# Optimization experiments

Hardware: AMD Instinct MI355X
Metric: run time of the kernel (lower is better)

## Reference

```python
import jax, jax.numpy as jnp
import numpy as np

B, T_IN, T_OUT = 32, 512, 800
N_MEL, ENC, ARNN, DRNN, PRE, ATT, LOCF, LOCK = 80, 512, 1024, 1024, 256, 128, 32, 31


def setup_inputs() -> dict:
    key = jax.random.key(0)
    ks = jax.random.split(key, 24)
    s = 0.02
    d = {
        'memory': jax.random.normal(ks[0], (B, T_IN, ENC), jnp.float32),
        'decoder_inputs': jax.random.normal(ks[1], (B, N_MEL, T_OUT), jnp.float32),
        'prenet_w1': jax.random.normal(ks[2], (PRE, N_MEL)) * s,
        'prenet_w2': jax.random.normal(ks[3], (PRE, PRE)) * s,
        'att_rnn_wih': jax.random.normal(ks[4], (4 * ARNN, PRE + ENC)) * s,
        'att_rnn_whh': jax.random.normal(ks[5], (4 * ARNN, ARNN)) * s,
        'att_rnn_bih': jnp.zeros((4 * ARNN,)),
        'att_rnn_bhh': jnp.zeros((4 * ARNN,)),
        'q_w': jax.random.normal(ks[6], (ATT, ARNN)) * s,
        'mem_w': jax.random.normal(ks[7], (ATT, ENC)) * s,
        'v_w': jax.random.normal(ks[8], (1, ATT)) * s,
        'loc_conv_w': jax.random.normal(ks[9], (LOCF, 2, LOCK)) * s,
        'loc_lin_w': jax.random.normal(ks[10], (ATT, LOCF)) * s,
        'dec_rnn_wih': jax.random.normal(ks[11], (4 * DRNN, ARNN + ENC)) * s,
        'dec_rnn_whh': jax.random.normal(ks[12], (4 * DRNN, DRNN)) * s,
        'dec_rnn_bih': jnp.zeros((4 * DRNN,)),
        'dec_rnn_bhh': jnp.zeros((4 * DRNN,)),
        'proj_w': jax.random.normal(ks[13], (N_MEL, DRNN + ENC)) * s,
        'proj_b': jnp.zeros((N_MEL,)),
        'gate_w': jax.random.normal(ks[14], (1, DRNN + ENC)) * s,
        'gate_b': jnp.zeros((1,)),
    }
    lengths = jax.random.randint(ks[15], (B,), T_IN // 2, T_IN + 1)
    d['memory_lengths'] = lengths.at[0].set(T_IN)  # ensure max length spans memory
    return d


def _lstm_cell(x, h, c, wih, whh, bih, bhh):
    z = x @ wih.T + bih + h @ whh.T + bhh
    i, f, g, o = jnp.split(z, 4, axis=-1)
    c = jax.nn.sigmoid(f) * c + jax.nn.sigmoid(i) * jnp.tanh(g)
    h = jax.nn.sigmoid(o) * jnp.tanh(c)
    return h, c


def reference(memory, decoder_inputs, prenet_w1, prenet_w2,
              att_rnn_wih, att_rnn_whh, att_rnn_bih, att_rnn_bhh,
              q_w, mem_w, v_w, loc_conv_w, loc_lin_w,
              dec_rnn_wih, dec_rnn_whh, dec_rnn_bih, dec_rnn_bhh,
              proj_w, proj_b, gate_w, gate_b, memory_lengths):
    # teacher-forced inputs: go frame + first T_OUT-1 mel frames -> [T_OUT, B, N_MEL]
    frames = jnp.transpose(decoder_inputs, (2, 0, 1))  # [T_OUT, B, N_MEL]
    dec_in = jnp.concatenate([jnp.zeros((1, B, N_MEL), memory.dtype), frames[:-1]], 0)
    # prenet (dropout omitted for deterministic reference)
    x = jax.nn.relu(dec_in @ prenet_w1.T)
    pren = jax.nn.relu(x @ prenet_w2.T)  # [T_OUT, B, PRE]

    pmem = memory @ mem_w.T  # [B, T_IN, ATT]
    valid = jnp.arange(T_IN)[None, :] < memory_lengths[:, None]  # [B, T_IN]

    def step(carry, dec_t):
        ah, ac, dh, dc, aw, awc, actx = carry
        cell_in = jnp.concatenate([dec_t, actx], -1)
        ah, ac = _lstm_cell(cell_in, ah, ac, att_rnn_wih, att_rnn_whh, att_rnn_bih, att_rnn_bhh)
        # location-sensitive attention
        cat = jnp.stack([aw, awc], axis=1)  # [B, 2, T_IN]
        loc = jax.lax.conv_general_dilated(cat, loc_conv_w, (1,), 'SAME',
                                           dimension_numbers=('NCH', 'OIH', 'NCH'))  # [B, LOCF, T_IN]
        loc = jnp.einsum('bct,ac->bta', loc, loc_lin_w)  # [B, T_IN, ATT]
        pq = (ah @ q_w.T)[:, None, :]  # [B, 1, ATT]
        energies = jnp.einsum('bta,a->bt', jnp.tanh(pq + loc + pmem), v_w[0])
        energies = jnp.where(valid, energies, -1e9)
        aw = jax.nn.softmax(energies, axis=1)
        actx = jnp.einsum('bt,btd->bd', aw, memory)
        awc = awc + aw
        din = jnp.concatenate([ah, actx], -1)
        dh, dc = _lstm_cell(din, dh, dc, dec_rnn_wih, dec_rnn_whh, dec_rnn_bih, dec_rnn_bhh)
        dhac = jnp.concatenate([dh, actx], -1)
        mel = dhac @ proj_w.T + proj_b  # [B, N_MEL]
        gate = (dhac @ gate_w.T + gate_b)[:, 0]  # [B]
        return (ah, ac, dh, dc, aw, awc, actx), (mel, gate, aw)

    z = lambda *s: jnp.zeros(s, memory.dtype)
    carry0 = (z(B, ARNN), z(B, ARNN), z(B, DRNN), z(B, DRNN), z(B, T_IN), z(B, T_IN), z(B, ENC))
    _, (mels, gates, aligns) = jax.lax.scan(step, carry0, pren)
    mel_outputs = jnp.transpose(mels, (1, 2, 0))      # [B, N_MEL, T_OUT]
    gate_outputs = jnp.transpose(gates, (1, 0))       # [B, T_OUT]
    alignments = jnp.transpose(aligns, (1, 0, 2))     # [B, T_OUT, T_IN]
    return mel_outputs, gate_outputs, alignments
```

## Files before the change

### kernel.cpp

```cpp
#include <hip/hip_runtime.h>
#include <cstddef>


constexpr size_t WT_ATT = 0;
constexpr size_t WT_DEC = 7340032;
constexpr size_t PREN_O = 17825792;
constexpr size_t PMEMT  = 24379392;
constexpr size_t W1T    = 26476544;
constexpr size_t W2T    = 26497024;
constexpr size_t QWT    = 26562560;
constexpr size_t PWT    = 26693632;
constexpr size_t MEMWT  = 26841088;
constexpr size_t XATT   = 26906624;
constexpr size_t XDEC   = 27021312;
constexpr size_t AH_O   = 27185152;
constexpr size_t AC_O   = 27217920;
constexpr size_t DH_O   = 27250688;
constexpr size_t DC_O   = 27283456;
constexpr size_t AWC_O  = 27316224;
constexpr size_t ACTX_O = 27348992;
constexpr size_t ENER_O = 27381760;
constexpr size_t LOC_O  = 27398144;
constexpr size_t BAR_O  = 27922432;

constexpr size_t MEL_OUT = 0;
constexpr size_t GATE_OUT = 2048000;
constexpr size_t ALIGN_OUT = 2073600;

__device__ __forceinline__ float gload(const float* p_) {
  return __hip_atomic_load(p_, __ATOMIC_RELAXED, __HIP_MEMORY_SCOPE_AGENT);
}
__device__ __forceinline__ void gstore(float* p_, float v) {
  __hip_atomic_store(p_, v, __ATOMIC_RELAXED, __HIP_MEMORY_SCOPE_AGENT);
}

__device__ __forceinline__ void gsync(float* ws, unsigned& epoch) {
  unsigned* cnt = (unsigned*)(ws + BAR_O);
  unsigned* rel = (unsigned*)(ws + BAR_O) + 128;
  __syncthreads();
  const int tid = threadIdx.x, bid = blockIdx.x;
  ++epoch;
  if (tid == 0)
    __hip_atomic_fetch_add(&cnt[(bid & 15) * 8], 1u, __ATOMIC_RELAXED,
                           __HIP_MEMORY_SCOPE_AGENT);
  if (bid == 0) {
    if (tid < 64) {
      const unsigned tgt = epoch * 32u;
      bool done;
      do {
        unsigned v = (tid < 16) ? __hip_atomic_load(&cnt[tid * 8], __ATOMIC_RELAXED,
                                                    __HIP_MEMORY_SCOPE_AGENT)
                                : tgt;
        done = v >= tgt;
        if (!done) __builtin_amdgcn_s_sleep(2);
      } while (__ballot(done) != ~0ull);
      for (int rr = tid; rr < 512; rr += 64)
        __hip_atomic_store(&rel[rr * 8], epoch, __ATOMIC_RELAXED,
                           __HIP_MEMORY_SCOPE_AGENT);
    }
  } else if (tid == 0) {
    while (__hip_atomic_load(&rel[bid * 8], __ATOMIC_RELAXED,
                             __HIP_MEMORY_SCOPE_AGENT) < epoch)
      __builtin_amdgcn_s_sleep(4);
  }
  __syncthreads();
}

__device__ __forceinline__ float sigf(float x) {
  float cx = fminf(fmaxf(x, -30.f), 30.f);
  return 1.f / (1.f + __expf(-cx));
}
__device__ __forceinline__ float tanh_f(float x) {
  float cx = fminf(fmaxf(x, -15.f), 15.f);
  float e = __expf(2.f * cx);
  return (e - 1.f) / (e + 1.f);
}

__device__ __forceinline__ void fused_block(
    const float* __restrict__ X, const int K, const float* __restrict__ WB,
    const int g, const int hh, const float* __restrict__ bih,
    const float* __restrict__ bhh, float* __restrict__ cst,
    float* __restrict__ d0, const int s0, float* __restrict__ d1, const int s1,
    float* __restrict__ d2, const int s2, const int tid,
    float* __restrict__ sm) {
  float* Xs = sm;
  float* Ws = sm + 2560;
  const int cg = tid & 3, bg = (tid >> 2) & 1, ks = tid >> 3;
  float acc[8][8];
#pragma unroll
  for (int ci = 0; ci < 8; ++ci)
#pragma unroll
    for (int bi = 0; bi < 8; ++bi) acc[ci][bi] = 0.f;

  const int nc = K >> 7;
  const int kloc = tid & 127, brow = tid >> 7;
  const float* xb = X + (size_t)brow * K + kloc;
  float px[8];
  float4 pw[4];
#pragma unroll
  for (int i = 0; i < 8; ++i) px[i] = gload(xb + (size_t)(2 * i) * K);
#pragma unroll
  for (int j = 0; j < 4; ++j)
    pw[j] = *(const float4*)(WB + (size_t)tid * 4 + j * 1024);

#pragma unroll 1
  for (int c = 0; c < nc; ++c) {
    __syncthreads();
#pragma unroll
    for (int i = 0; i < 8; ++i) Xs[kloc * 20 + brow + 2 * i] = px[i];
#pragma unroll
    for (int j = 0; j < 4; ++j) {
      const int ff = tid + 256 * j;
      *(float4*)(Ws + (ff >> 3) * 36 + (ff & 7) * 4) = pw[j];
    }
    __syncthreads();
    if (c + 1 < nc) {
      const float* xb2 = xb + (c + 1) * 128;
#pragma unroll
      for (int i = 0; i < 8; ++i) px[i] = gload(xb2 + (size_t)(2 * i) * K);
      const float* wb2 = WB + (size_t)(c + 1) * 4096 + (size_t)tid * 4;
#pragma unroll
      for (int j = 0; j < 4; ++j) pw[j] = *(const float4*)(wb2 + j * 1024);
    }
#pragma unroll
    for (int i = 0; i < 4; ++i) {
      const int k = i * 32 + ks;
      const float4 wA = *(const float4*)(Ws + k * 36 + cg * 8);
      const float4 wBv = *(const float4*)(Ws + k * 36 + cg * 8 + 4);
      const float4 xA = *(const float4*)(Xs + k * 20 + bg * 8);
      const float4 xBv = *(const float4*)(Xs + k * 20 + bg * 8 + 4);
      const float wr[8] = {wA.x, wA.y, wA.z, wA.w, wBv.x, wBv.y, wBv.z, wBv.w};
      const float xr[8] = {xA.x, xA.y, xA.z, xA.w, xBv.x, xBv.y, xBv.z, xBv.w};
#pragma unroll
      for (int ci = 0; ci < 8; ++ci)
#pragma unroll
        for (int bi = 0; bi < 8; ++bi)
          acc[ci][bi] = fmaf(wr[ci], xr[bi], acc[ci][bi]);
    }
  }
#pragma unroll
  for (int ci = 0; ci < 8; ++ci)
#pragma unroll
    for (int bi = 0; bi < 8; ++bi) {
      float v = acc[ci][bi];
      v += __shfl_xor(v, 8);
      v += __shfl_xor(v, 16);
      v += __shfl_xor(v, 32);
      acc[ci][bi] = v;
    }
  __syncthreads();
  float* red = sm;
  float* zs = sm + 2560;
  const int lane = tid & 63, wv = tid >> 6;
  if (lane < 8) {
#pragma unroll
    for (int ci = 0; ci < 8; ++ci)
#pragma unroll
      for (int bi = 0; bi < 8; ++bi)
        red[((bg * 8 + bi) * 32 + cg * 8 + ci) * 5 + wv] = acc[ci][bi];
  }
  __syncthreads();
#pragma unroll
  for (int m = 0; m < 2; ++m) {
    const int o = tid + 256 * m;
    zs[o] = red[o * 5] + red[o * 5 + 1] + red[o * 5 + 2] + red[o * 5 + 3];
  }
  __syncthreads();
  if (tid < 128) {
    const int bb = tid & 15, jj = tid >> 4;
    const int j = g * 8 + jj;
    const int b = hh * 16 + bb;
    const float zi = zs[bb * 32 + jj] + bih[j] + bhh[j];
    const float zf = zs[bb * 32 + 8 + jj] + bih[1024 + j] + bhh[1024 + j];
    const float zg = zs[bb * 32 + 16 + jj] + bih[2048 + j] + bhh[2048 + j];
    const float zo = zs[bb * 32 + 24 + jj] + bih[3072 + j] + bhh[3072 + j];
    const float cp = cst[(size_t)b * 1024 + j];
    const float ct = sigf(zf) * cp + sigf(zi) * tanh_f(zg);
    const float ho = sigf(zo) * tanh_f(ct);
    cst[(size_t)b * 1024 + j] = ct;
    gstore(d0 + (size_t)b * s0 + j, ho);
    if (d1) gstore(d1 + (size_t)b * s1 + j, ho);
    if (d2) gstore(d2 + (size_t)b * s2 + j, ho);
  }
}

__global__ __launch_bounds__(256) void k_small(
    const float* __restrict__ w1, const float* __restrict__ w2,
    const float* __restrict__ qw, const float* __restrict__ memw,
    const float* __restrict__ projw, const float* __restrict__ gatew,
    float* __restrict__ ws) {
  size_t i = (size_t)blockIdx.x * 256 + threadIdx.x;
  if (i < 20480) { size_t j = i & 255, m = i >> 8; ws[W1T + m * 256 + j] = w1[j * 80 + m]; return; }
  i -= 20480;
  if (i < 65536) { size_t j = i & 255, k = i >> 8; ws[W2T + k * 256 + j] = w2[j * 256 + k]; return; }
  i -= 65536;
  if (i < 131072) { size_t j = i & 127, k = i >> 7; ws[QWT + k * 128 + j] = qw[j * 1024 + k]; return; }
  i -= 131072;
  if (i < 65536) { size_t a = i & 127, e = i >> 7; ws[MEMWT + e * 128 + a] = memw[a * 512 + e]; return; }
  i -= 65536;
  if (i < 147456) {
    size_t o = i % 96, k = i / 96;
    float v = 0.f;
    if (o < 80) v = projw[o * 1536 + k];
    else if (o == 80) v = gatew[k];
    ws[PWT + k * 96 + o] = v;
  }
}

__device__ __forceinline__ size_t att_out(int gcol, int kout) {
  const int gate = gcol >> 10, g = (gcol & 1023) >> 3, jj = gcol & 7;
  return WT_ATT + ((size_t)g * 1792 + kout) * 32 + gate * 8 + jj;
}
__device__ __forceinline__ size_t dec_out(int gcol, int kout) {
  const int gate = gcol >> 10, g = (gcol & 1023) >> 3, jj = gcol & 7;
  return WT_DEC + ((size_t)g * 2560 + kout) * 32 + gate * 8 + jj;
}
__global__ __launch_bounds__(256) void k_tr_a_wih(const float* __restrict__ w,
                                                  float* __restrict__ ws) {
  const int i = blockIdx.x * 256 + threadIdx.x;
  const int gcol = i / 768, k = i - gcol * 768;
  ws[att_out(gcol, k)] = w[i];
}
__global__ __launch_bounds__(256) void k_tr_a_whh(const float* __restrict__ w,
                                                  float* __restrict__ ws) {
  const int i = blockIdx.x * 256 + threadIdx.x;
  const int gcol = i >> 10, kin = i & 1023;
  ws[att_out(gcol, 768 + kin)] = w[i];
}
__global__ __launch_bounds__(256) void k_tr_d_wih(const float* __restrict__ w,
                                                  float* __restrict__ ws) {
  const int i = blockIdx.x * 256 + threadIdx.x;
  const int gcol = i / 1536, kin = i - gcol * 1536;
  const int kout = (kin < 1024) ? kin : kin + 1024;
  ws[dec_out(gcol, kout)] = w[i];
}
__global__ __launch_bounds__(256) void k_tr_d_whh(const float* __restrict__ w,
                                                  float* __restrict__ ws) {
  const int i = blockIdx.x * 256 + threadIdx.x;
  const int gcol = i >> 10, kin = i & 1023;
  ws[dec_out(gcol, 1024 + kin)] = w[i];
}

__global__ __launch_bounds__(256) void k_prenet(const float* __restrict__ din,
                                                float* __restrict__ ws) {
  __shared__ float h1[8][257];
  const int tg = blockIdx.x, b = blockIdx.y, j = threadIdx.x;
  float acc[8] = {0, 0, 0, 0, 0, 0, 0, 0};
  for (int m = 0; m < 80; ++m) {
    const float w = ws[W1T + m * 256 + j];
#pragma unroll
    for (int q = 0; q < 8; ++q) {
      const int t = tg * 8 + q;
      const float x = (t > 0) ? din[((size_t)b * 80 + m) * 800 + (t - 1)] : 0.f;
      acc[q] = fmaf(x, w, acc[q]);
    }
  }
#pragma unroll
  for (int q = 0; q < 8; ++q) h1[q][j] = fmaxf(acc[q], 0.f);
  __syncthreads();
  float a2[8] = {0, 0, 0, 0, 0, 0, 0, 0};
  for (int k = 0; k < 256; ++k) {
    const float w = ws[W2T + k * 256 + j];
#pragma unroll
    for (int q = 0; q < 8; ++q) a2[q] = fmaf(h1[q][k], w, a2[q]);
  }
#pragma unroll
  for (int q = 0; q < 8; ++q) {
    const int t = tg * 8 + q;
    ws[PREN_O + ((size_t)t * 32 + b) * 256 + j] = fmaxf(a2[q], 0.f);
  }
}

__global__ __launch_bounds__(256) void k_pmem(const float* __restrict__ mem,
                                              float* __restrict__ ws) {
  __shared__ float mt[16 * 516];
  const int b = blockIdx.x, tc = blockIdx.y, tid = threadIdx.x;
  const int ti0 = tc * 16;
  for (int i = tid; i < 16 * 128; i += 256) {
    const int r = i >> 7, c = i & 127;
    *(float4*)(mt + r * 516 + c * 4) =
        *(const float4*)(mem + ((size_t)b * 512 + ti0 + r) * 512 + c * 4);
  }
  __syncthreads();
  const int a = tid & 127, th = tid >> 7;
  float acc[8] = {0, 0, 0, 0, 0, 0, 0, 0};
  for (int e = 0; e < 512; ++e) {
    const float w = ws[MEMWT + (size_t)e * 128 + a];
#pragma unroll
    for (int q = 0; q < 8; ++q) acc[q] = fmaf(w, mt[(th * 8 + q) * 516 + e], acc[q]);
  }
#pragma unroll
  for (int q = 0; q < 8; ++q)
    ws[PMEMT + ((size_t)b * 128 + a) * 512 + ti0 + th * 8 + q] = acc[q];
}

struct TP {
  const float *mem, *abih, *abhh, *lconv, *llw, *vw, *dbih, *dbhh, *projb, *gateb;
  const int* lens;
  float* ws;
  float* out;
};

__global__ __launch_bounds__(256, 2) void taco_main(TP p) {
  __shared__ float smem[7168];
  float* const ws = p.ws;
  unsigned epoch = 0;
  const int bid = blockIdx.x, tid = threadIdx.x;
  const int r = bid & 255, hh = bid >> 8;

#pragma unroll 1
  for (int t = 0; t <= 800; ++t) {
    const int par = t & 1, nxt = (t + 1) & 1, prv = (t - 1) & 1;
    if (r < 128) {
      if (t < 800)
        fused_block(ws + XATT + (size_t)par * 57344 + (size_t)hh * 16 * 1792,
                    1792, ws + WT_ATT + (size_t)r * 1792 * 32, r, hh,
                    p.abih, p.abhh, ws + AC_O,
                    ws + AH_O, 1024,
                    ws + XATT + (size_t)nxt * 57344 + 768, 1792,
                    ws + XDEC + (size_t)par * 81920, 2560, tid, smem);
    } else {
      if (t > 0)
        fused_block(ws + XDEC + (size_t)prv * 81920 + (size_t)hh * 16 * 2560,
                    2560, ws + WT_DEC + (size_t)(r - 128) * 2560 * 32, r - 128,
                    hh, p.dbih, p.dbhh, ws + DC_O,
                    ws + DH_O, 1024,
                    ws + XDEC + (size_t)par * 81920 + 1024, 2560,
                    nullptr, 0, tid, smem);
    }
    gsync(ws, epoch);

    if (r < 128) {
      if (t < 800) {
        const int b = r >> 2, q8 = ((r & 3) << 1) | hh;
        float* sa = smem;
        float* sloc = smem + 1024;
        float* pqp = smem + 3136;
        float* pq = smem + 3392;
        float* sme = smem + 3520;
#pragma unroll
        for (int i = 0; i < 4; ++i)
          sa[tid + 256 * i] = gload(ws + AH_O + (size_t)b * 1024 + tid + 256 * i);
#pragma unroll
        for (int ii = 0; ii < 8; ++ii) {
          const int flat = tid + 256 * ii;
          sloc[(flat >> 5) * 33 + (flat & 31)] =
              gload(ws + LOC_O + (size_t)b * 16384 + (size_t)q8 * 2048 + flat);
        }
        __syncthreads();
        {
          const int j = tid & 127, kh = tid >> 7;
          const float* qb = ws + QWT + (size_t)kh * 512 * 128 + j;
          const float* ab = sa + kh * 512;
          float a0 = 0, a1 = 0, a2 = 0, a3 = 0;
          for (int k = 0; k < 512; k += 4) {
            a0 = fmaf(qb[(size_t)k * 128], ab[k], a0);
            a1 = fmaf(qb[(size_t)(k + 1) * 128], ab[k + 1], a1);
            a2 = fmaf(qb[(size_t)(k + 2) * 128], ab[k + 2], a2);
            a3 = fmaf(qb[(size_t)(k + 3) * 128], ab[k + 3], a3);
          }
          pqp[tid] = (a0 + a1) + (a2 + a3);
        }
        __syncthreads();
        if (tid < 128) pq[tid] = pqp[tid] + pqp[128 + tid];
        __syncthreads();
        const int ti_l = tid & 63, th = tid >> 6;
        float lr[32];
#pragma unroll
        for (int f = 0; f < 32; ++f) lr[f] = sloc[ti_l * 33 + f];
        const float* pmb = ws + PMEMT + (size_t)b * 65536 +
                           (size_t)(th * 32) * 512 + q8 * 64 + ti_l;
        float acc_e = 0;
#pragma unroll 2
        for (int a0 = 0; a0 < 32; ++a0) {
          const int a = th * 32 + a0;
          float s = pq[a] + pmb[(size_t)a0 * 512];
          const float* la = p.llw + a * 32;
#pragma unroll
          for (int f = 0; f < 32; ++f) s = fmaf(lr[f], la[f], s);
          acc_e = fmaf(p.vw[a], tanh_f(s), acc_e);
        }
        sme[tid] = acc_e;
        __syncthreads();
        if (tid < 64) {
          const int ti = q8 * 64 + tid;
          const float e = sme[tid] + sme[64 + tid] + sme[128 + tid] + sme[192 + tid];
          gstore(ws + ENER_O + (size_t)b * 512 + ti, (ti < p.lens[b]) ? e : -1e9f);
        }
      }
    } else if (r < 160 && hh == 0) {
      if (t > 0) {
        const int b = r - 128;
        float* sx = smem;
        float* sred = smem + 1536;
#pragma unroll
        for (int i = 0; i < 6; ++i) {
          const int flat = tid + 256 * i;
          sx[flat] = (flat < 1024)
                         ? gload(ws + DH_O + (size_t)b * 1024 + flat)
                         : gload(ws + ACTX_O + (size_t)prv * 16384 + (size_t)b * 512 +
                                 (flat - 1024));
        }
        __syncthreads();
        float p0 = 0.f, p1 = 0.f, p2 = 0.f, p3 = 0.f;
        const int o = tid / 3, ks2 = tid - o * 3;
        if (o < 81) {
          const float* wcol = ws + PWT + o;
          const int k0 = ks2 * 512;
          for (int k = k0; k < k0 + 512; k += 4) {
            p0 = fmaf(sx[k], wcol[(size_t)k * 96], p0);
            p1 = fmaf(sx[k + 1], wcol[(size_t)(k + 1) * 96], p1);
            p2 = fmaf(sx[k + 2], wcol[(size_t)(k + 2) * 96], p2);
            p3 = fmaf(sx[k + 3], wcol[(size_t)(k + 3) * 96], p3);
          }
        }
        sred[tid] = (p0 + p1) + (p2 + p3);
        __syncthreads();
        if (tid < 81) {
          float ssum = sred[tid * 3] + sred[tid * 3 + 1] + sred[tid * 3 + 2];
          ssum += (tid < 80) ? p.projb[tid] : p.gateb[0];
          if (tid < 80)
            p.out[MEL_OUT + ((size_t)b * 80 + tid) * 800 + (t - 1)] = ssum;
          else
            p.out[GATE_OUT + (size_t)b * 800 + (t - 1)] = ssum;
        }
      }
    }
    gsync(ws, epoch);

    if (t < 800) {
      const int b = r >> 3, dc16 = ((r & 7) << 1) | hh;
      float* se = smem;
      float* red = smem + 512;
      float* sp = smem + 768;
      float* sc = smem + 1280;
      float* saw = smem + 1536;
      float* sawh = smem + 1600;
      float* slc = smem + 1664;
      se[tid] = gload(ws + ENER_O + (size_t)b * 512 + tid);
      se[256 + tid] = gload(ws + ENER_O + (size_t)b * 512 + 256 + tid);
      for (int i = tid; i < 1984; i += 256) slc[i] = p.lconv[i];
      __syncthreads();
      red[tid] = fmaxf(se[tid], se[256 + tid]);
      __syncthreads();
      for (int s = 128; s > 0; s >>= 1) {
        if (tid < s) red[tid] = fmaxf(red[tid], red[tid + s]);
        __syncthreads();
      }
      const float mx = red[0];
      __syncthreads();
      const float p0 = __expf(se[tid] - mx), p1 = __expf(se[256 + tid] - mx);
      sp[tid] = p0;
      sp[256 + tid] = p1;
      red[tid] = p0 + p1;
      __syncthreads();
      for (int s = 128; s > 0; s >>= 1) {
        if (tid < s) red[tid] += red[tid + s];
        __syncthreads();
      }
      const float inv = 1.f / red[0];
      const int tseg = tid >> 5, dl = tid & 31;
      const int base = dc16 * 32;
      const float* mrow =
          p.mem + ((size_t)b * 512 + tseg * 64) * 512 + base + dl;
      float ca = 0, cb = 0;
      for (int i = 0; i < 64; i += 2) {
        ca = fmaf(sp[tseg * 64 + i], mrow[(size_t)i * 512], ca);
        cb = fmaf(sp[tseg * 64 + i + 1], mrow[(size_t)(i + 1) * 512], cb);
      }
      sc[tid] = ca + cb;
      for (int i = tid; i < 62; i += 256) {
        const int x = base - 15 + i;
        const bool ok = (unsigned)x < 512u;
        const float awx = ok ? sp[x] * inv : 0.f;
        saw[i] = awx;
        sawh[i] = awx + (ok ? gload(ws + AWC_O + (size_t)par * 16384 +
                                    (size_t)b * 512 + x)
                            : 0.f);
      }
      __syncthreads();
      if (tid < 32) {
        float v = sc[tid] + sc[32 + tid] + sc[64 + tid] + sc[96 + tid] +
                  sc[128 + tid] + sc[160 + tid] + sc[192 + tid] + sc[224 + tid];
        v *= inv;
        const int dd = base + tid;
        gstore(ws + ACTX_O + (size_t)par * 16384 + (size_t)b * 512 + dd, v);
        gstore(ws + XATT + (size_t)nxt * 57344 + (size_t)b * 1792 + 256 + dd, v);
        gstore(ws + XDEC + (size_t)par * 81920 + (size_t)b * 2560 + 2048 + dd, v);
        gstore(ws + AWC_O + (size_t)nxt * 16384 + (size_t)b * 512 + dd,
               sawh[15 + tid]);
        p.out[ALIGN_OUT + ((size_t)b * 800 + t) * 512 + dd] = sp[dd] * inv;
      }
      if (t + 1 < 800) {
        const int f = tid & 31, tig = tid >> 5;
#pragma unroll 2
        for (int tt = 0; tt < 4; ++tt) {
          const int til = tig + tt * 8;
          float a2 = 0;
#pragma unroll
          for (int k2 = 0; k2 < 31; ++k2) a2 = fmaf(saw[til + k2], slc[f * 62 + k2], a2);
#pragma unroll
          for (int k2 = 0; k2 < 31; ++k2)
            a2 = fmaf(sawh[til + k2], slc[f * 62 + 31 + k2], a2);
          gstore(ws + LOC_O + (size_t)b * 16384 + (size_t)(base + til) * 32 + f, a2);
        }
        if (dc16 < 8 && tid < 32) {
          const int cc = dc16 * 32 + tid;
          gstore(ws + XATT + (size_t)nxt * 57344 + (size_t)b * 1792 + cc,
                 ws[PREN_O + ((size_t)(t + 1) * 32 + b) * 256 + cc]);
        }
      }
    }
    gsync(ws, epoch);
  }
}

extern "C" void kernel_launch(void* const* d_in, const int* in_sizes, int n_in,
                              void* d_out, int out_size, void* d_ws, size_t ws_size,
                              hipStream_t stream) {
  (void)in_sizes; (void)n_in; (void)out_size; (void)ws_size;
  const float* mem = (const float*)d_in[0];
  const float* decin = (const float*)d_in[1];
  const float* w1 = (const float*)d_in[2];
  const float* w2 = (const float*)d_in[3];
  const float* awih = (const float*)d_in[4];
  const float* awhh = (const float*)d_in[5];
  const float* abih = (const float*)d_in[6];
  const float* abhh = (const float*)d_in[7];
  const float* qw = (const float*)d_in[8];
  const float* memw = (const float*)d_in[9];
  const float* vw = (const float*)d_in[10];
  const float* lconv = (const float*)d_in[11];
  const float* llw = (const float*)d_in[12];
  const float* dwih = (const float*)d_in[13];
  const float* dwhh = (const float*)d_in[14];
  const float* dbih = (const float*)d_in[15];
  const float* dbhh = (const float*)d_in[16];
  const float* projw = (const float*)d_in[17];
  const float* projb = (const float*)d_in[18];
  const float* gatew = (const float*)d_in[19];
  const float* gateb = (const float*)d_in[20];
  const int* lens = (const int*)d_in[21];
  float* ws = (float*)d_ws;
  float* out = (float*)d_out;

  hipMemsetAsync(ws + XATT, 0, (114688 + 163840) * sizeof(float), stream);
  hipMemsetAsync(ws + AH_O, 0, 737280 * sizeof(float), stream);
  hipMemsetAsync(ws + BAR_O, 0, 4224 * sizeof(unsigned), stream);

  k_small<<<1680, 256, 0, stream>>>(w1, w2, qw, memw, projw, gatew, ws);
  k_tr_a_wih<<<12288, 256, 0, stream>>>(awih, ws);
  k_tr_a_whh<<<16384, 256, 0, stream>>>(awhh, ws);
  k_tr_d_wih<<<24576, 256, 0, stream>>>(dwih, ws);
  k_tr_d_whh<<<16384, 256, 0, stream>>>(dwhh, ws);
  k_prenet<<<dim3(100, 32), 256, 0, stream>>>(decin, ws);
  k_pmem<<<dim3(32, 32), 256, 0, stream>>>(mem, ws);

  TP tp{mem, abih, abhh, lconv, llw, vw, dbih, dbhh, projb, gateb, lens, ws, out};
  taco_main<<<512, 256, 0, stream>>>(tp);
}
```

Measured before the change: 131.8 ms.

## Split persistent decoder grid across 1024 blocks with quarter-batch work per block

Doubles the persistent kernel's grid from 512 to 1024 blocks and halves each block's share of work. The LSTM GEMM tiles now cover 8 batch rows instead of 16, and the attention energy and context windows shrink to 32 and 16 elements. Launch bounds rise to 4 blocks per CU with less shared memory, and the grid barrier counters are re-strided for 32 groups and 1024 release slots. The aim is more parallelism per serial timestep so that each step's latency drops, at the cost of a more expensive global barrier and less weight reuse, since every weight tile is now streamed by twice as many blocks.

After: 176.0 ms. 1.34x slower.

```diff
diff --git a/kernel.cpp b/kernel.cpp
--- a/kernel.cpp
+++ b/kernel.cpp
@@ -41,25 +41,25 @@
   const int tid = threadIdx.x, bid = blockIdx.x;
   ++epoch;
   if (tid == 0)
-    __hip_atomic_fetch_add(&cnt[(bid & 15) * 8], 1u, __ATOMIC_RELAXED,
+    __hip_atomic_fetch_add(&cnt[(bid & 31) * 4], 1u, __ATOMIC_RELAXED,
                            __HIP_MEMORY_SCOPE_AGENT);
   if (bid == 0) {
     if (tid < 64) {
       const unsigned tgt = epoch * 32u;
       bool done;
       do {
-        unsigned v = (tid < 16) ? __hip_atomic_load(&cnt[tid * 8], __ATOMIC_RELAXED,
+        unsigned v = (tid < 32) ? __hip_atomic_load(&cnt[tid * 4], __ATOMIC_RELAXED,
                                                     __HIP_MEMORY_SCOPE_AGENT)
                                 : tgt;
         done = v >= tgt;
         if (!done) __builtin_amdgcn_s_sleep(2);
       } while (__ballot(done) != ~0ull);
-      for (int rr = tid; rr < 512; rr += 64)
-        __hip_atomic_store(&rel[rr * 8], epoch, __ATOMIC_RELAXED,
+      for (int rr = tid; rr < 1024; rr += 64)
+        __hip_atomic_store(&rel[rr * 4], epoch, __ATOMIC_RELAXED,
                            __HIP_MEMORY_SCOPE_AGENT);
     }
   } else if (tid == 0) {
-    while (__hip_atomic_load(&rel[bid * 8], __ATOMIC_RELAXED,
+    while (__hip_atomic_load(&rel[bid * 4], __ATOMIC_RELAXED,
                              __HIP_MEMORY_SCOPE_AGENT) < epoch)
       __builtin_amdgcn_s_sleep(4);
   }
@@ -78,27 +78,27 @@
 
 __device__ __forceinline__ void fused_block(
     const float* __restrict__ X, const int K, const float* __restrict__ WB,
-    const int g, const int hh, const float* __restrict__ bih,
+    const int g, const int q4, const float* __restrict__ bih,
     const float* __restrict__ bhh, float* __restrict__ cst,
     float* __restrict__ d0, const int s0, float* __restrict__ d1, const int s1,
     float* __restrict__ d2, const int s2, const int tid,
     float* __restrict__ sm) {
   float* Xs = sm;
-  float* Ws = sm + 2560;
+  float* Ws = sm + 1536;
   const int cg = tid & 3, bg = (tid >> 2) & 1, ks = tid >> 3;
-  float acc[8][8];
+  float acc[8][4];
 #pragma unroll
   for (int ci = 0; ci < 8; ++ci)
 #pragma unroll
-    for (int bi = 0; bi < 8; ++bi) acc[ci][bi] = 0.f;
+    for (int bi = 0; bi < 4; ++bi) acc[ci][bi] = 0.f;
 
   const int nc = K >> 7;
   const int kloc = tid & 127, brow = tid >> 7;
-  const float* xb = X + (size_t)brow * K + kloc;
-  float px[8];
+  const float* xb = X + (size_t)(brow * 4) * K + kloc;
+  float px[4];
   float4 pw[4];
 #pragma unroll
-  for (int i = 0; i < 8; ++i) px[i] = gload(xb + (size_t)(2 * i) * K);
+  for (int i = 0; i < 4; ++i) px[i] = gload(xb + (size_t)i * K);
 #pragma unroll
   for (int j = 0; j < 4; ++j)
     pw[j] = *(const float4*)(WB + (size_t)tid * 4 + j * 1024);
@@ -106,8 +106,8 @@
 #pragma unroll 1
   for (int c = 0; c < nc; ++c) {
     __syncthreads();
-#pragma unroll
-    for (int i = 0; i < 8; ++i) Xs[kloc * 20 + brow + 2 * i] = px[i];
+    *(float4*)(Xs + kloc * 12 + brow * 4) =
+        make_float4(px[0], px[1], px[2], px[3]);
 #pragma unroll
     for (int j = 0; j < 4; ++j) {
       const int ff = tid + 256 * j;
@@ -117,7 +117,7 @@
     if (c + 1 < nc) {
       const float* xb2 = xb + (c + 1) * 128;
 #pragma unroll
-      for (int i = 0; i < 8; ++i) px[i] = gload(xb2 + (size_t)(2 * i) * K);
+      for (int i = 0; i < 4; ++i) px[i] = gload(xb2 + (size_t)i * K);
       const float* wb2 = WB + (size_t)(c + 1) * 4096 + (size_t)tid * 4;
 #pragma unroll
       for (int j = 0; j < 4; ++j) pw[j] = *(const float4*)(wb2 + j * 1024);
@@ -127,21 +127,20 @@
       const int k = i * 32 + ks;
       const float4 wA = *(const float4*)(Ws + k * 36 + cg * 8);
       const float4 wBv = *(const float4*)(Ws + k * 36 + cg * 8 + 4);
-      const float4 xA = *(const float4*)(Xs + k * 20 + bg * 8);
-      const float4 xBv = *(const float4*)(Xs + k * 20 + bg * 8 + 4);
+      const float4 xA = *(const float4*)(Xs + k * 12 + bg * 4);
       const float wr[8] = {wA.x, wA.y, wA.z, wA.w, wBv.x, wBv.y, wBv.z, wBv.w};
-      const float xr[8] = {xA.x, xA.y, xA.z, xA.w, xBv.x, xBv.y, xBv.z, xBv.w};
+      const float xr[4] = {xA.x, xA.y, xA.z, xA.w};
 #pragma unroll
       for (int ci = 0; ci < 8; ++ci)
 #pragma unroll
-        for (int bi = 0; bi < 8; ++bi)
+        for (int bi = 0; bi < 4; ++bi)
           acc[ci][bi] = fmaf(wr[ci], xr[bi], acc[ci][bi]);
     }
   }
 #pragma unroll
   for (int ci = 0; ci < 8; ++ci)
 #pragma unroll
-    for (int bi = 0; bi < 8; ++bi) {
+    for (int bi = 0; bi < 4; ++bi) {
       float v = acc[ci][bi];
       v += __shfl_xor(v, 8);
       v += __shfl_xor(v, 16);
@@ -150,26 +149,25 @@
     }
   __syncthreads();
   float* red = sm;
-  float* zs = sm + 2560;
+  float* zs = sm + 1280;
   const int lane = tid & 63, wv = tid >> 6;
   if (lane < 8) {
 #pragma unroll
     for (int ci = 0; ci < 8; ++ci)
 #pragma unroll
-      for (int bi = 0; bi < 8; ++bi)
-        red[((bg * 8 + bi) * 32 + cg * 8 + ci) * 5 + wv] = acc[ci][bi];
-  }
-  __syncthreads();
-#pragma unroll
-  for (int m = 0; m < 2; ++m) {
-    const int o = tid + 256 * m;
+      for (int bi = 0; bi < 4; ++bi)
+        red[((bg * 4 + bi) * 32 + cg * 8 + ci) * 5 + wv] = acc[ci][bi];
+  }
+  __syncthreads();
+  {
+    const int o = tid;
     zs[o] = red[o * 5] + red[o * 5 + 1] + red[o * 5 + 2] + red[o * 5 + 3];
   }
   __syncthreads();
-  if (tid < 128) {
-    const int bb = tid & 15, jj = tid >> 4;
+  if (tid < 64) {
+    const int bb = tid & 7, jj = tid >> 3;
     const int j = g * 8 + jj;
-    const int b = hh * 16 + bb;
+    const int b = q4 * 8 + bb;
     const float zi = zs[bb * 32 + jj] + bih[j] + bhh[j];
     const float zf = zs[bb * 32 + 8 + jj] + bih[1024 + j] + bhh[1024 + j];
     const float zg = zs[bb * 32 + 16 + jj] + bih[2048 + j] + bhh[2048 + j];
@@ -301,29 +299,29 @@
   float* out;
 };
 
-__global__ __launch_bounds__(256, 2) void taco_main(TP p) {
-  __shared__ float smem[7168];
+__global__ __launch_bounds__(256, 4) void taco_main(TP p) {
+  __shared__ float smem[6144];
   float* const ws = p.ws;
   unsigned epoch = 0;
   const int bid = blockIdx.x, tid = threadIdx.x;
-  const int r = bid & 255, hh = bid >> 8;
+  const int r = bid & 255, q4 = bid >> 8;
 
 #pragma unroll 1
   for (int t = 0; t <= 800; ++t) {
     const int par = t & 1, nxt = (t + 1) & 1, prv = (t - 1) & 1;
     if (r < 128) {
       if (t < 800)
-        fused_block(ws + XATT + (size_t)par * 57344 + (size_t)hh * 16 * 1792,
-                    1792, ws + WT_ATT + (size_t)r * 1792 * 32, r, hh,
+        fused_block(ws + XATT + (size_t)par * 57344 + (size_t)q4 * 8 * 1792,
+                    1792, ws + WT_ATT + (size_t)r * 1792 * 32, r, q4,
                     p.abih, p.abhh, ws + AC_O,
                     ws + AH_O, 1024,
                     ws + XATT + (size_t)nxt * 57344 + 768, 1792,
                     ws + XDEC + (size_t)par * 81920, 2560, tid, smem);
     } else {
       if (t > 0)
-        fused_block(ws + XDEC + (size_t)prv * 81920 + (size_t)hh * 16 * 2560,
+        fused_block(ws + XDEC + (size_t)prv * 81920 + (size_t)q4 * 8 * 2560,
                     2560, ws + WT_DEC + (size_t)(r - 128) * 2560 * 32, r - 128,
-                    hh, p.dbih, p.dbhh, ws + DC_O,
+                    q4, p.dbih, p.dbhh, ws + DC_O,
                     ws + DH_O, 1024,
                     ws + XDEC + (size_t)par * 81920 + 1024, 2560,
                     nullptr, 0, tid, smem);
@@ -332,20 +330,20 @@
 
     if (r < 128) {
       if (t < 800) {
-        const int b = r >> 2, q8 = ((r & 3) << 1) | hh;
+        const int b = r >> 2, sub = ((r & 3) << 2) | q4;
         float* sa = smem;
         float* sloc = smem + 1024;
-        float* pqp = smem + 3136;
-        float* pq = smem + 3392;
-        float* sme = smem + 3520;
+        float* pqp = smem + 2080;
+        float* pq = smem + 2336;
+        float* sme = smem + 2464;
 #pragma unroll
         for (int i = 0; i < 4; ++i)
           sa[tid + 256 * i] = gload(ws + AH_O + (size_t)b * 1024 + tid + 256 * i);
 #pragma unroll
-        for (int ii = 0; ii < 8; ++ii) {
+        for (int ii = 0; ii < 4; ++ii) {
           const int flat = tid + 256 * ii;
           sloc[(flat >> 5) * 33 + (flat & 31)] =
-              gload(ws + LOC_O + (size_t)b * 16384 + (size_t)q8 * 2048 + flat);
+              gload(ws + LOC_O + (size_t)b * 16384 + (size_t)sub * 1024 + flat);
         }
         __syncthreads();
         {
@@ -364,16 +362,16 @@
         __syncthreads();
         if (tid < 128) pq[tid] = pqp[tid] + pqp[128 + tid];
         __syncthreads();
-        const int ti_l = tid & 63, th = tid >> 6;
+        const int ti_l = tid & 31, th = tid >> 5;
         float lr[32];
 #pragma unroll
         for (int f = 0; f < 32; ++f) lr[f] = sloc[ti_l * 33 + f];
         const float* pmb = ws + PMEMT + (size_t)b * 65536 +
-                           (size_t)(th * 32) * 512 + q8 * 64 + ti_l;
+                           (size_t)(th * 16) * 512 + sub * 32 + ti_l;
         float acc_e = 0;
 #pragma unroll 2
-        for (int a0 = 0; a0 < 32; ++a0) {
-          const int a = th * 32 + a0;
+        for (int a0 = 0; a0 < 16; ++a0) {
+          const int a = th * 16 + a0;
           float s = pq[a] + pmb[(size_t)a0 * 512];
           const float* la = p.llw + a * 32;
 #pragma unroll
@@ -382,13 +380,15 @@
         }
         sme[tid] = acc_e;
         __syncthreads();
-        if (tid < 64) {
-          const int ti = q8 * 64 + tid;
-          const float e = sme[tid] + sme[64 + tid] + sme[128 + tid] + sme[192 + tid];
+        if (tid < 32) {
+          const int ti = sub * 32 + tid;
+          float e = sme[tid];
+#pragma unroll
+          for (int i = 1; i < 8; ++i) e += sme[i * 32 + tid];
           gstore(ws + ENER_O + (size_t)b * 512 + ti, (ti < p.lens[b]) ? e : -1e9f);
         }
       }
-    } else if (r < 160 && hh == 0) {
+    } else if (r < 160 && q4 == 0) {
       if (t > 0) {
         const int b = r - 128;
         float* sx = smem;
@@ -429,14 +429,14 @@
     gsync(ws, epoch);
 
     if (t < 800) {
-      const int b = r >> 3, dc16 = ((r & 7) << 1) | hh;
+      const int b = r >> 3, win = ((r & 7) << 2) | q4;
       float* se = smem;
       float* red = smem + 512;
       float* sp = smem + 768;
       float* sc = smem + 1280;
       float* saw = smem + 1536;
-      float* sawh = smem + 1600;
-      float* slc = smem + 1664;
+      float* sawh = smem + 1584;
+      float* slc = smem + 1632;
       se[tid] = gload(ws + ENER_O + (size_t)b * 512 + tid);
       se[256 + tid] = gload(ws + ENER_O + (size_t)b * 512 + 256 + tid);
       for (int i = tid; i < 1984; i += 256) slc[i] = p.lconv[i];
@@ -459,17 +459,17 @@
         __syncthreads();
       }
       const float inv = 1.f / red[0];
-      const int tseg = tid >> 5, dl = tid & 31;
-      const int base = dc16 * 32;
+      const int tseg = tid >> 4, dl = tid & 15;
+      const int base = win * 16;
       const float* mrow =
-          p.mem + ((size_t)b * 512 + tseg * 64) * 512 + base + dl;
+          p.mem + ((size_t)b * 512 + tseg * 32) * 512 + base + dl;
       float ca = 0, cb = 0;
-      for (int i = 0; i < 64; i += 2) {
-        ca = fmaf(sp[tseg * 64 + i], mrow[(size_t)i * 512], ca);
-        cb = fmaf(sp[tseg * 64 + i + 1], mrow[(size_t)(i + 1) * 512], cb);
+      for (int i = 0; i < 32; i += 2) {
+        ca = fmaf(sp[tseg * 32 + i], mrow[(size_t)i * 512], ca);
+        cb = fmaf(sp[tseg * 32 + i + 1], mrow[(size_t)(i + 1) * 512], cb);
       }
       sc[tid] = ca + cb;
-      for (int i = tid; i < 62; i += 256) {
+      for (int i = tid; i < 46; i += 256) {
         const int x = base - 15 + i;
         const bool ok = (unsigned)x < 512u;
         const float awx = ok ? sp[x] * inv : 0.f;
@@ -479,9 +479,10 @@
                             : 0.f);
       }
       __syncthreads();
-      if (tid < 32) {
-        float v = sc[tid] + sc[32 + tid] + sc[64 + tid] + sc[96 + tid] +
-                  sc[128 + tid] + sc[160 + tid] + sc[192 + tid] + sc[224 + tid];
+      if (tid < 16) {
+        float v = 0.f;
+#pragma unroll
+        for (int s = 0; s < 16; ++s) v += sc[s * 16 + tid];
         v *= inv;
         const int dd = base + tid;
         gstore(ws + ACTX_O + (size_t)par * 16384 + (size_t)b * 512 + dd, v);
@@ -489,12 +490,12 @@
         gstore(ws + XDEC + (size_t)par * 81920 + (size_t)b * 2560 + 2048 + dd, v);
         gstore(ws + AWC_O + (size_t)nxt * 16384 + (size_t)b * 512 + dd,
                sawh[15 + tid]);
-        p.out[ALIGN_OUT + ((size_t)b * 800 + t) * 512 + dd] = sp[dd] * inv;
+      p.out[ALIGN_OUT + ((size_t)b * 800 + t) * 512 + dd] = sp[dd] * inv;
       }
       if (t + 1 < 800) {
         const int f = tid & 31, tig = tid >> 5;
 #pragma unroll 2
-        for (int tt = 0; tt < 4; ++tt) {
+        for (int tt = 0; tt < 2; ++tt) {
           const int til = tig + tt * 8;
           float a2 = 0;
 #pragma unroll
@@ -504,8 +505,8 @@
             a2 = fmaf(sawh[til + k2], slc[f * 62 + 31 + k2], a2);
           gstore(ws + LOC_O + (size_t)b * 16384 + (size_t)(base + til) * 32 + f, a2);
         }
-        if (dc16 < 8 && tid < 32) {
-          const int cc = dc16 * 32 + tid;
+        if (win < 16 && tid < 16) {
+          const int cc = win * 16 + tid;
           gstore(ws + XATT + (size_t)nxt * 57344 + (size_t)b * 1792 + cc,
                  ws[PREN_O + ((size_t)(t + 1) * 32 + b) * 256 + cc]);
         }
@@ -557,5 +558,5 @@
   k_pmem<<<dim3(32, 32), 256, 0, stream>>>(mem, ws);
 
   TP tp{mem, abih, abhh, lconv, llw, vw, dbih, dbhh, projb, gateb, lens, ws, out};
-  taco_main<<<512, 256, 0, stream>>>(tp);
-}
+  taco_main<<<1024, 256, 0, stream>>>(tp);
+}
```

## Split LSTM gate GEMMs into partial products computed in separate phases across 768 blocks

Applied to the files above, without the earlier changes.

Restructures the persistent kernel from 512 to 768 blocks in three groups. The LSTM gate matmuls are split into partial sums by input segment (prenet/context, attention hidden, decoder hidden), computed in whichever phase their inputs are ready and stored to workspace, so the critical-path step after each barrier does a smaller GEMM. The per-step concatenated input buffers are dropped in favour of reading sources directly, and the attention-context and location-conv work is regrouped onto 64-wide slices. The cost is extra global traffic for the partial gate sums, more blocks taking part in each grid barrier, and reuse of weight-transpose workspace regions (W1T/MEMWT) as scratch, which assumes those weights are no longer needed once the main loop starts.

Result: slower. 161.3 ms (+22.4%).

```diff
diff --git a/kernel.cpp b/kernel.cpp
--- a/kernel.cpp
+++ b/kernel.cpp
@@ -11,8 +11,8 @@
 constexpr size_t QWT    = 26562560;
 constexpr size_t PWT    = 26693632;
 constexpr size_t MEMWT  = 26841088;
-constexpr size_t XATT   = 26906624;
-constexpr size_t XDEC   = 27021312;
+constexpr size_t ZDEC0  = 26906624;
+constexpr size_t ZDEC1  = 27037696;
 constexpr size_t AH_O   = 27185152;
 constexpr size_t AC_O   = 27217920;
 constexpr size_t DH_O   = 27250688;
@@ -27,6 +27,11 @@
 constexpr size_t GATE_OUT = 2048000;
 constexpr size_t ALIGN_OUT = 2073600;
 
+__device__ __forceinline__ float* zatt_ptr(float* ws, int b) {
+  return ws + (b < 21 ? (size_t)W1T + (size_t)b * 4096
+                      : (size_t)MEMWT + (size_t)(b - 21) * 4096);
+}
+
 __device__ __forceinline__ float gload(const float* p_) {
   return __hip_atomic_load(p_, __ATOMIC_RELAXED, __HIP_MEMORY_SCOPE_AGENT);
 }
@@ -41,25 +46,25 @@
   const int tid = threadIdx.x, bid = blockIdx.x;
   ++epoch;
   if (tid == 0)
-    __hip_atomic_fetch_add(&cnt[(bid & 15) * 8], 1u, __ATOMIC_RELAXED,
+    __hip_atomic_fetch_add(&cnt[(bid & 31) * 4], 1u, __ATOMIC_RELAXED,
                            __HIP_MEMORY_SCOPE_AGENT);
   if (bid == 0) {
     if (tid < 64) {
-      const unsigned tgt = epoch * 32u;
+      const unsigned tgt = epoch * 24u;
       bool done;
       do {
-        unsigned v = (tid < 16) ? __hip_atomic_load(&cnt[tid * 8], __ATOMIC_RELAXED,
+        unsigned v = (tid < 32) ? __hip_atomic_load(&cnt[tid * 4], __ATOMIC_RELAXED,
                                                     __HIP_MEMORY_SCOPE_AGENT)
                                 : tgt;
         done = v >= tgt;
         if (!done) __builtin_amdgcn_s_sleep(2);
       } while (__ballot(done) != ~0ull);
-      for (int rr = tid; rr < 512; rr += 64)
-        __hip_atomic_store(&rel[rr * 8], epoch, __ATOMIC_RELAXED,
+      for (int rr = tid; rr < 768; rr += 64)
+        __hip_atomic_store(&rel[rr * 4], epoch, __ATOMIC_RELAXED,
                            __HIP_MEMORY_SCOPE_AGENT);
     }
   } else if (tid == 0) {
-    while (__hip_atomic_load(&rel[bid * 8], __ATOMIC_RELAXED,
+    while (__hip_atomic_load(&rel[bid * 4], __ATOMIC_RELAXED,
                              __HIP_MEMORY_SCOPE_AGENT) < epoch)
       __builtin_amdgcn_s_sleep(4);
   }
@@ -76,13 +81,15 @@
   return (e - 1.f) / (e + 1.f);
 }
 
-__device__ __forceinline__ void fused_block(
-    const float* __restrict__ X, const int K, const float* __restrict__ WB,
-    const int g, const int hh, const float* __restrict__ bih,
-    const float* __restrict__ bhh, float* __restrict__ cst,
-    float* __restrict__ d0, const int s0, float* __restrict__ d1, const int s1,
-    float* __restrict__ d2, const int s2, const int tid,
-    float* __restrict__ sm) {
+__device__ __forceinline__ void fused2(
+    float* __restrict__ ws,
+    const float* __restrict__ XA, const int sA, const int ncA,
+    const float* __restrict__ XB, const int sB,
+    const int nc, const float* __restrict__ WB,
+    const int mode, const int g, const int b0, const int t,
+    const float* __restrict__ bih, const float* __restrict__ bhh,
+    float* __restrict__ cst, float* __restrict__ d0,
+    const int tid, float* __restrict__ sm) {
   float* Xs = sm;
   float* Ws = sm + 2560;
   const int cg = tid & 3, bg = (tid >> 2) & 1, ks = tid >> 3;
@@ -92,13 +99,14 @@
 #pragma unroll
     for (int bi = 0; bi < 8; ++bi) acc[ci][bi] = 0.f;
 
-  const int nc = K >> 7;
   const int kloc = tid & 127, brow = tid >> 7;
-  const float* xb = X + (size_t)brow * K + kloc;
   float px[8];
   float4 pw[4];
-#pragma unroll
-  for (int i = 0; i < 8; ++i) px[i] = gload(xb + (size_t)(2 * i) * K);
+  {
+#pragma unroll
+    for (int i = 0; i < 8; ++i)
+      px[i] = gload(XA + (size_t)(brow + 2 * i) * sA + kloc);
+  }
 #pragma unroll
   for (int j = 0; j < 4; ++j)
     pw[j] = *(const float4*)(WB + (size_t)tid * 4 + j * 1024);
@@ -115,10 +123,15 @@
     }
     __syncthreads();
     if (c + 1 < nc) {
-      const float* xb2 = xb + (c + 1) * 128;
-#pragma unroll
-      for (int i = 0; i < 8; ++i) px[i] = gload(xb2 + (size_t)(2 * i) * K);
-      const float* wb2 = WB + (size_t)(c + 1) * 4096 + (size_t)tid * 4;
+      const int c2 = c + 1;
+      const bool inA = c2 < ncA;
+      const float* base = inA ? XA : XB;
+      const int st = inA ? sA : sB;
+      const int ko = (inA ? c2 : c2 - ncA) * 128;
+#pragma unroll
+      for (int i = 0; i < 8; ++i)
+        px[i] = gload(base + (size_t)(brow + 2 * i) * st + ko + kloc);
+      const float* wb2 = WB + (size_t)c2 * 4096 + (size_t)tid * 4;
 #pragma unroll
       for (int j = 0; j < 4; ++j) pw[j] = *(const float4*)(wb2 + j * 1024);
     }
@@ -166,21 +179,48 @@
     zs[o] = red[o * 5] + red[o * 5 + 1] + red[o * 5 + 2] + red[o * 5 + 3];
   }
   __syncthreads();
+  if (mode <= 2) {
+#pragma unroll
+    for (int m = 0; m < 2; ++m) {
+      const int o = tid + 256 * m, bb = o >> 5, cp = o & 31, b = b0 + bb;
+      float* dst = (mode == 2)
+                       ? (zatt_ptr(ws, b) + (size_t)g * 32 + cp)
+                       : (ws + (mode ? ZDEC1 : ZDEC0) + (size_t)b * 4096 +
+                          (size_t)g * 32 + cp);
+      gstore(dst, zs[o]);
+    }
+    return;
+  }
   if (tid < 128) {
     const int bb = tid & 15, jj = tid >> 4;
     const int j = g * 8 + jj;
-    const int b = hh * 16 + bb;
-    const float zi = zs[bb * 32 + jj] + bih[j] + bhh[j];
-    const float zf = zs[bb * 32 + 8 + jj] + bih[1024 + j] + bhh[1024 + j];
-    const float zg = zs[bb * 32 + 16 + jj] + bih[2048 + j] + bhh[2048 + j];
-    const float zo = zs[bb * 32 + 24 + jj] + bih[3072 + j] + bhh[3072 + j];
+    const int b = b0 + bb;
+    float za0 = 0.f, za1 = 0.f, za2 = 0.f, za3 = 0.f;
+    if (mode == 3) {
+      if (t > 0) {
+        const float* zp = zatt_ptr(ws, b) + (size_t)g * 32 + jj;
+        za0 = gload(zp);
+        za1 = gload(zp + 8);
+        za2 = gload(zp + 16);
+        za3 = gload(zp + 24);
+      }
+    } else {
+      const float* z0 = ws + ZDEC0 + (size_t)b * 4096 + (size_t)g * 32 + jj;
+      const float* z1 = ws + ZDEC1 + (size_t)b * 4096 + (size_t)g * 32 + jj;
+      za0 = gload(z0) + gload(z1);
+      za1 = gload(z0 + 8) + gload(z1 + 8);
+      za2 = gload(z0 + 16) + gload(z1 + 16);
+      za3 = gload(z0 + 24) + gload(z1 + 24);
+    }
+    const float zi = zs[bb * 32 + jj] + za0 + bih[j] + bhh[j];
+    const float zf = zs[bb * 32 + 8 + jj] + za1 + bih[1024 + j] + bhh[1024 + j];
+    const float zg = zs[bb * 32 + 16 + jj] + za2 + bih[2048 + j] + bhh[2048 + j];
+    const float zo = zs[bb * 32 + 24 + jj] + za3 + bih[3072 + j] + bhh[3072 + j];
     const float cp = cst[(size_t)b * 1024 + j];
     const float ct = sigf(zf) * cp + sigf(zi) * tanh_f(zg);
     const float ho = sigf(zo) * tanh_f(ct);
     cst[(size_t)b * 1024 + j] = ct;
-    gstore(d0 + (size_t)b * s0 + j, ho);
-    if (d1) gstore(d1 + (size_t)b * s1 + j, ho);
-    if (d2) gstore(d2 + (size_t)b * s2 + j, ho);
+    gstore(d0 + (size_t)b * 1024 + j, ho);
   }
 }
 
@@ -301,38 +341,42 @@
   float* out;
 };
 
-__global__ __launch_bounds__(256, 2) void taco_main(TP p) {
+__global__ __launch_bounds__(256, 3) void taco_main(TP p) {
   __shared__ float smem[7168];
   float* const ws = p.ws;
   unsigned epoch = 0;
   const int bid = blockIdx.x, tid = threadIdx.x;
-  const int r = bid & 255, hh = bid >> 8;
+  const int grp = bid >> 8, r = bid & 255;
 
 #pragma unroll 1
   for (int t = 0; t <= 800; ++t) {
     const int par = t & 1, nxt = (t + 1) & 1, prv = (t - 1) & 1;
-    if (r < 128) {
-      if (t < 800)
-        fused_block(ws + XATT + (size_t)par * 57344 + (size_t)hh * 16 * 1792,
-                    1792, ws + WT_ATT + (size_t)r * 1792 * 32, r, hh,
-                    p.abih, p.abhh, ws + AC_O,
-                    ws + AH_O, 1024,
-                    ws + XATT + (size_t)nxt * 57344 + 768, 1792,
-                    ws + XDEC + (size_t)par * 81920, 2560, tid, smem);
-    } else {
-      if (t > 0)
-        fused_block(ws + XDEC + (size_t)prv * 81920 + (size_t)hh * 16 * 2560,
-                    2560, ws + WT_DEC + (size_t)(r - 128) * 2560 * 32, r - 128,
-                    hh, p.dbih, p.dbhh, ws + DC_O,
-                    ws + DH_O, 1024,
-                    ws + XDEC + (size_t)par * 81920 + 1024, 2560,
-                    nullptr, 0, tid, smem);
+    if (grp == 0) {
+      if (t < 800) {
+        const int g = r >> 1, hh = r & 1, b0 = hh * 16;
+        fused2(ws,
+               ws + PREN_O + ((size_t)t * 32 + b0) * 256, 256, 2,
+               ws + ACTX_O + (size_t)prv * 16384 + (size_t)b0 * 512, 512,
+               6, ws + WT_ATT + (size_t)g * 1792 * 32,
+               3, g, b0, t, p.abih, p.abhh, ws + AC_O, ws + AH_O,
+               tid, smem);
+      }
+    } else if (grp == 1) {
+      if (t > 0) {
+        const int g = r >> 1, hh = r & 1, b0 = hh * 16;
+        fused2(ws,
+               ws + ACTX_O + (size_t)prv * 16384 + (size_t)b0 * 512, 512, 4,
+               nullptr, 0,
+               4, ws + WT_DEC + (size_t)g * 2560 * 32 + (size_t)2048 * 32,
+               4, g, b0, t, p.dbih, p.dbhh, ws + DC_O, ws + DH_O,
+               tid, smem);
+      }
     }
     gsync(ws, epoch);
 
-    if (r < 128) {
-      if (t < 800) {
-        const int b = r >> 2, q8 = ((r & 3) << 1) | hh;
+    if (t < 800) {
+      if (grp == 0) {
+        const int b = r >> 3, q8 = r & 7;
         float* sa = smem;
         float* sloc = smem + 1024;
         float* pqp = smem + 3136;
@@ -387,56 +431,31 @@
           const float e = sme[tid] + sme[64 + tid] + sme[128 + tid] + sme[192 + tid];
           gstore(ws + ENER_O + (size_t)b * 512 + ti, (ti < p.lens[b]) ? e : -1e9f);
         }
-      }
-    } else if (r < 160 && hh == 0) {
-      if (t > 0) {
-        const int b = r - 128;
-        float* sx = smem;
-        float* sred = smem + 1536;
-#pragma unroll
-        for (int i = 0; i < 6; ++i) {
-          const int flat = tid + 256 * i;
-          sx[flat] = (flat < 1024)
-                         ? gload(ws + DH_O + (size_t)b * 1024 + flat)
-                         : gload(ws + ACTX_O + (size_t)prv * 16384 + (size_t)b * 512 +
-                                 (flat - 1024));
-        }
-        __syncthreads();
-        float p0 = 0.f, p1 = 0.f, p2 = 0.f, p3 = 0.f;
-        const int o = tid / 3, ks2 = tid - o * 3;
-        if (o < 81) {
-          const float* wcol = ws + PWT + o;
-          const int k0 = ks2 * 512;
-          for (int k = k0; k < k0 + 512; k += 4) {
-            p0 = fmaf(sx[k], wcol[(size_t)k * 96], p0);
-            p1 = fmaf(sx[k + 1], wcol[(size_t)(k + 1) * 96], p1);
-            p2 = fmaf(sx[k + 2], wcol[(size_t)(k + 2) * 96], p2);
-            p3 = fmaf(sx[k + 3], wcol[(size_t)(k + 3) * 96], p3);
-          }
-        }
-        sred[tid] = (p0 + p1) + (p2 + p3);
-        __syncthreads();
-        if (tid < 81) {
-          float ssum = sred[tid * 3] + sred[tid * 3 + 1] + sred[tid * 3 + 2];
-          ssum += (tid < 80) ? p.projb[tid] : p.gateb[0];
-          if (tid < 80)
-            p.out[MEL_OUT + ((size_t)b * 80 + tid) * 800 + (t - 1)] = ssum;
-          else
-            p.out[GATE_OUT + (size_t)b * 800 + (t - 1)] = ssum;
-        }
+      } else if (grp == 1) {
+        const int g = r >> 1, hh = r & 1, b0 = hh * 16;
+        fused2(ws, ws + AH_O + (size_t)b0 * 1024, 1024, 8, nullptr, 0, 8,
+               ws + WT_DEC + (size_t)g * 2560 * 32,
+               0, g, b0, t, nullptr, nullptr, nullptr, nullptr,
+               tid, smem);
+      } else {
+        const int g = r >> 1, hh = r & 1, b0 = hh * 16;
+        fused2(ws, ws + DH_O + (size_t)b0 * 1024, 1024, 8, nullptr, 0, 8,
+               ws + WT_DEC + (size_t)g * 2560 * 32 + (size_t)1024 * 32,
+               1, g, b0, t, nullptr, nullptr, nullptr, nullptr,
+               tid, smem);
       }
     }
     gsync(ws, epoch);
 
-    if (t < 800) {
-      const int b = r >> 3, dc16 = ((r & 7) << 1) | hh;
+    if (grp == 1 && t < 800) {
+      const int b = r >> 3, dc8 = r & 7;
       float* se = smem;
       float* red = smem + 512;
       float* sp = smem + 768;
       float* sc = smem + 1280;
       float* saw = smem + 1536;
-      float* sawh = smem + 1600;
-      float* slc = smem + 1664;
+      float* sawh = smem + 1664;
+      float* slc = smem + 1792;
       se[tid] = gload(ws + ENER_O + (size_t)b * 512 + tid);
       se[256 + tid] = gload(ws + ENER_O + (size_t)b * 512 + 256 + tid);
       for (int i = tid; i < 1984; i += 256) slc[i] = p.lconv[i];
@@ -459,17 +478,16 @@
         __syncthreads();
       }
       const float inv = 1.f / red[0];
-      const int tseg = tid >> 5, dl = tid & 31;
-      const int base = dc16 * 32;
-      const float* mrow =
-          p.mem + ((size_t)b * 512 + tseg * 64) * 512 + base + dl;
+      const int tseg = tid >> 6, dl = tid & 63;
+      const int base = dc8 * 64;
+      const float* mrow = p.mem + ((size_t)b * 512 + tseg * 128) * 512 + base + dl;
       float ca = 0, cb = 0;
-      for (int i = 0; i < 64; i += 2) {
-        ca = fmaf(sp[tseg * 64 + i], mrow[(size_t)i * 512], ca);
-        cb = fmaf(sp[tseg * 64 + i + 1], mrow[(size_t)(i + 1) * 512], cb);
+      for (int i = 0; i < 128; i += 2) {
+        ca = fmaf(sp[tseg * 128 + i], mrow[(size_t)i * 512], ca);
+        cb = fmaf(sp[tseg * 128 + i + 1], mrow[(size_t)(i + 1) * 512], cb);
       }
       sc[tid] = ca + cb;
-      for (int i = tid; i < 62; i += 256) {
+      for (int i = tid; i < 95; i += 256) {
         const int x = base - 15 + i;
         const bool ok = (unsigned)x < 512u;
         const float awx = ok ? sp[x] * inv : 0.f;
@@ -479,22 +497,18 @@
                             : 0.f);
       }
       __syncthreads();
-      if (tid < 32) {
-        float v = sc[tid] + sc[32 + tid] + sc[64 + tid] + sc[96 + tid] +
-                  sc[128 + tid] + sc[160 + tid] + sc[192 + tid] + sc[224 + tid];
-        v *= inv;
+      if (tid < 64) {
+        const float v = (sc[tid] + sc[64 + tid] + sc[128 + tid] + sc[192 + tid]) * inv;
         const int dd = base + tid;
         gstore(ws + ACTX_O + (size_t)par * 16384 + (size_t)b * 512 + dd, v);
-        gstore(ws + XATT + (size_t)nxt * 57344 + (size_t)b * 1792 + 256 + dd, v);
-        gstore(ws + XDEC + (size_t)par * 81920 + (size_t)b * 2560 + 2048 + dd, v);
         gstore(ws + AWC_O + (size_t)nxt * 16384 + (size_t)b * 512 + dd,
                sawh[15 + tid]);
         p.out[ALIGN_OUT + ((size_t)b * 800 + t) * 512 + dd] = sp[dd] * inv;
       }
       if (t + 1 < 800) {
         const int f = tid & 31, tig = tid >> 5;
-#pragma unroll 2
-        for (int tt = 0; tt < 4; ++tt) {
+#pragma unroll 1
+        for (int tt = 0; tt < 8; ++tt) {
           const int til = tig + tt * 8;
           float a2 = 0;
 #pragma unroll
@@ -504,11 +518,47 @@
             a2 = fmaf(sawh[til + k2], slc[f * 62 + 31 + k2], a2);
           gstore(ws + LOC_O + (size_t)b * 16384 + (size_t)(base + til) * 32 + f, a2);
         }
-        if (dc16 < 8 && tid < 32) {
-          const int cc = dc16 * 32 + tid;
-          gstore(ws + XATT + (size_t)nxt * 57344 + (size_t)b * 1792 + cc,
-                 ws[PREN_O + ((size_t)(t + 1) * 32 + b) * 256 + cc]);
+      }
+    } else if (grp == 2 && t + 1 < 800) {
+      const int g = r >> 1, hh = r & 1, b0 = hh * 16;
+      fused2(ws, ws + AH_O + (size_t)b0 * 1024, 1024, 8, nullptr, 0, 8,
+             ws + WT_ATT + (size_t)g * 1792 * 32 + (size_t)768 * 32,
+             2, g, b0, t, nullptr, nullptr, nullptr, nullptr,
+             tid, smem);
+    } else if (grp == 0 && r < 32 && t > 0) {
+      const int b = r;
+      float* sx = smem;
+      float* sred = smem + 1536;
+#pragma unroll
+      for (int i = 0; i < 6; ++i) {
+        const int flat = tid + 256 * i;
+        sx[flat] = (flat < 1024)
+                       ? gload(ws + DH_O + (size_t)b * 1024 + flat)
+                       : gload(ws + ACTX_O + (size_t)prv * 16384 + (size_t)b * 512 +
+                               (flat - 1024));
+      }
+      __syncthreads();
+      float p0 = 0.f, p1 = 0.f, p2 = 0.f, p3 = 0.f;
+      const int o = tid / 3, ks2 = tid - o * 3;
+      if (o < 81) {
+        const float* wcol = ws + PWT + o;
+        const int k0 = ks2 * 512;
+        for (int k = k0; k < k0 + 512; k += 4) {
+          p0 = fmaf(sx[k], wcol[(size_t)k * 96], p0);
+          p1 = fmaf(sx[k + 1], wcol[(size_t)(k + 1) * 96], p1);
+          p2 = fmaf(sx[k + 2], wcol[(size_t)(k + 2) * 96], p2);
+          p3 = fmaf(sx[k + 3], wcol[(size_t)(k + 3) * 96], p3);
         }
+      }
+      sred[tid] = (p0 + p1) + (p2 + p3);
+      __syncthreads();
+      if (tid < 81) {
+        float ssum = sred[tid * 3] + sred[tid * 3 + 1] + sred[tid * 3 + 2];
+        ssum += (tid < 80) ? p.projb[tid] : p.gateb[0];
+        if (tid < 80)
+          p.out[MEL_OUT + ((size_t)b * 80 + tid) * 800 + (t - 1)] = ssum;
+        else
+          p.out[GATE_OUT + (size_t)b * 800 + (t - 1)] = ssum;
       }
     }
     gsync(ws, epoch);
@@ -544,7 +594,7 @@
   float* ws = (float*)d_ws;
   float* out = (float*)d_out;
 
-  hipMemsetAsync(ws + XATT, 0, (114688 + 163840) * sizeof(float), stream);
+  hipMemsetAsync(ws + ZDEC0, 0, 278528 * sizeof(float), stream);
   hipMemsetAsync(ws + AH_O, 0, 737280 * sizeof(float), stream);
   hipMemsetAsync(ws + BAR_O, 0, 4224 * sizeof(unsigned), stream);
 
@@ -557,5 +607,5 @@
   k_pmem<<<dim3(32, 32), 256, 0, stream>>>(mem, ws);
 
   TP tp{mem, abih, abhh, lconv, llw, vw, dbih, dbhh, projb, gateb, lens, ws, out};
-  taco_main<<<512, 256, 0, stream>>>(tp);
-}
+  taco_main<<<768, 256, 0, stream>>>(tp);
+}
```
